# Kernel optimization log

Hardware: AMD Instinct MI355X
Metric: run time of the kernel (lower is better)

Reference implementation:

```python
import jax, jax.numpy as jnp
import numpy as np

BS, LQ = 16, 300
D, NH = 256, 8
HD = D // NH
NLAYERS, DFF = 6, 1024
NLVL, NPTS = 4, 4
SUMP = NLVL * NPTS  # total sampling points per head
SPATIAL = [(80, 80), (40, 40), (20, 20), (10, 10)]
LEN_V = sum(h * w for h, w in SPATIAL)  # 8500
OFFSET_SCALE = 0.5


def layer_norm(x, g, b, eps=1e-5):
    m = jnp.mean(x, -1, keepdims=True)
    v = jnp.mean((x - m) ** 2, -1, keepdims=True)
    return (x - m) * jax.lax.rsqrt(v + eps) * g + b


def bilinear_gather(v, loc, Hs, Ws):
    # v: [bs, nh, Hs*Ws, hd]; loc: [bs, nh, N, 2] in [0,1] (x, y)
    # grid_sample bilinear, align_corners=False, zero padding
    x = loc[..., 0] * Ws - 0.5
    y = loc[..., 1] * Hs - 0.5
    x0 = jnp.floor(x); y0 = jnp.floor(y)
    x1 = x0 + 1.0; y1 = y0 + 1.0
    wx1 = x - x0; wx0 = 1.0 - wx1
    wy1 = y - y0; wy0 = 1.0 - wy1

    def corner(xi, yi, w):
        valid = (xi >= 0) & (xi <= Ws - 1) & (yi >= 0) & (yi <= Hs - 1)
        idx = (jnp.clip(yi, 0, Hs - 1) * Ws + jnp.clip(xi, 0, Ws - 1)).astype(jnp.int32)
        g = jnp.take_along_axis(v, idx[..., None], axis=2)  # [bs,nh,N,hd]
        return g * (w * valid)[..., None]

    return (corner(x0, y0, wx0 * wy0) + corner(x1, y0, wx1 * wy0)
            + corner(x0, y1, wx0 * wy1) + corner(x1, y1, wx1 * wy1))


def ms_deform_attn(value, loc, attn_w):
    # value [bs,LenV,D]; loc [bs,Lq,nh,SUMP,2]; attn_w [bs,Lq,nh,SUMP]
    bs, Lq = loc.shape[:2]
    v = value.reshape(bs, -1, NH, HD).transpose(0, 2, 1, 3)  # [bs,nh,LenV,hd]
    sizes = [h * w for h, w in SPATIAL]
    offs = np.cumsum([0] + sizes)
    outs = []
    for lvl, (Hs, Ws) in enumerate(SPATIAL):
        v_l = v[:, :, offs[lvl]:offs[lvl + 1], :]
        loc_l = loc[:, :, :, lvl * NPTS:(lvl + 1) * NPTS, :]
        loc_l = loc_l.transpose(0, 2, 1, 3, 4).reshape(bs, NH, Lq * NPTS, 2)
        s = bilinear_gather(v_l, loc_l, Hs, Ws).reshape(bs, NH, Lq, NPTS, HD)
        outs.append(s)
    samp = jnp.concatenate(outs, axis=3)  # [bs,nh,Lq,SUMP,hd]
    w = attn_w.transpose(0, 2, 1, 3)[..., None]
    out = jnp.sum(samp * w, axis=3)  # [bs,nh,Lq,hd]
    return out.transpose(0, 2, 1, 3).reshape(bs, Lq, D)


def mha(q_in, k_in, v_in, Wqkv, bqkv, Wo, bo):
    # torch nn.MultiheadAttention (batch_first), no dropout, no mask
    bs, Lq, _ = q_in.shape
    Wq, Wk, Wv = jnp.split(Wqkv, 3, axis=0)
    bq, bk, bv = jnp.split(bqkv, 3)
    q = (q_in @ Wq.T + bq).reshape(bs, Lq, NH, HD)
    k = (k_in @ Wk.T + bk).reshape(bs, -1, NH, HD)
    v = (v_in @ Wv.T + bv).reshape(bs, -1, NH, HD)
    scores = jnp.einsum('bqhd,bkhd->bhqk', q, k) / jnp.sqrt(jnp.float32(HD))
    a = jax.nn.softmax(scores, axis=-1)
    o = jnp.einsum('bhqk,bkhd->bqhd', a, v).reshape(bs, Lq, D)
    return o @ Wo.T + bo


def _forward(target, reference_points, value, query_pos_embed,
             attn_Wqkv, attn_bqkv, attn_Wo, attn_bo, n1_g, n1_b,
             so_W, so_b, aw_W, aw_b, g_W, g_b, gn_g, gn_b,
             l1_W, l1_b, l2_W, l2_b, n3_g, n3_b):
    bs, Lq = target.shape[:2]
    # num_points_scale = 1/n_points per point (all levels use NPTS points)
    nps = jnp.full((SUMP, 1), 1.0 / NPTS, dtype=target.dtype)
    t = target
    for i in range(NLAYERS):
        # self-attention
        q = t + query_pos_embed
        t2 = mha(q, q, t, attn_Wqkv[i], attn_bqkv[i], attn_Wo[i], attn_bo[i])
        t = layer_norm(t + t2, n1_g[i], n1_b[i])
        # MS deformable cross-attention (4-dim reference_points branch)
        qc = t + query_pos_embed
        so = (qc @ so_W[i].T + so_b[i]).reshape(bs, Lq, NH, SUMP, 2)
        aw = jax.nn.softmax((qc @ aw_W[i].T + aw_b[i]).reshape(bs, Lq, NH, SUMP), axis=-1)
        ref = reference_points[:, :, None, None, :]  # [bs,Lq,1,1,4]
        loc = ref[..., :2] + so * nps * ref[..., 2:] * OFFSET_SCALE
        t2 = ms_deform_attn(value, loc, aw)
        # gateway fusion
        gates = jax.nn.sigmoid(jnp.concatenate([t, t2], -1) @ g_W[i].T + g_b[i])
        g1, g2 = jnp.split(gates, 2, axis=-1)
        t = layer_norm(g1 * t + g2 * t2, gn_g[i], gn_b[i])
        # FFN
        t2 = jax.nn.relu(t @ l1_W[i].T + l1_b[i]) @ l2_W[i].T + l2_b[i]
        t = layer_norm(jnp.clip(t + t2, -65504.0, 65504.0), n3_g[i], n3_b[i])
    return t


def setup_inputs() -> dict:
    key = jax.random.key(0)
    ks = iter(jax.random.split(key, 40))

    def rn(shape, s=0.02):
        return jax.random.normal(next(ks), shape, dtype=jnp.float32) * s

    inp = {
        'target': jax.random.normal(next(ks), (BS, LQ, D), dtype=jnp.float32),
        'reference_points': jax.random.uniform(next(ks), (BS, LQ, 4), dtype=jnp.float32) * 0.5 + 0.25,
        'value': jax.random.normal(next(ks), (BS, LEN_V, D), dtype=jnp.float32),
        'query_pos_embed': jax.random.normal(next(ks), (BS, LQ, D), dtype=jnp.float32),
        'attn_Wqkv': rn((NLAYERS, 3 * D, D)),
        'attn_bqkv': jnp.zeros((NLAYERS, 3 * D), jnp.float32),
        'attn_Wo': rn((NLAYERS, D, D)),
        'attn_bo': jnp.zeros((NLAYERS, D), jnp.float32),
        'n1_g': jnp.ones((NLAYERS, D), jnp.float32),
        'n1_b': jnp.zeros((NLAYERS, D), jnp.float32),
        'so_W': rn((NLAYERS, NH * SUMP * 2, D)),
        'so_b': rn((NLAYERS, NH * SUMP * 2), 0.5),
        'aw_W': rn((NLAYERS, NH * SUMP, D)),
        'aw_b': jnp.zeros((NLAYERS, NH * SUMP), jnp.float32),
        'g_W': rn((NLAYERS, 2 * D, 2 * D)),
        'g_b': jnp.zeros((NLAYERS, 2 * D), jnp.float32),
        'gn_g': jnp.ones((NLAYERS, D), jnp.float32),
        'gn_b': jnp.zeros((NLAYERS, D), jnp.float32),
        'l1_W': rn((NLAYERS, DFF, D)),
        'l1_b': jnp.zeros((NLAYERS, DFF), jnp.float32),
        'l2_W': rn((NLAYERS, D, DFF)),
        'l2_b': jnp.zeros((NLAYERS, D), jnp.float32),
        'n3_g': jnp.ones((NLAYERS, D), jnp.float32),
        'n3_b': jnp.zeros((NLAYERS, D), jnp.float32),
    }
    return inp


def reference(target, reference_points, value, query_pos_embed,
              attn_Wqkv, attn_bqkv, attn_Wo, attn_bo, n1_g, n1_b,
              so_W, so_b, aw_W, aw_b, g_W, g_b, gn_g, gn_b,
              l1_W, l1_b, l2_W, l2_b, n3_g, n3_b):
    return _forward(target, reference_points, value, query_pos_embed,
                    attn_Wqkv, attn_bqkv, attn_Wo, attn_bo, n1_g, n1_b,
                    so_W, so_b, aw_W, aw_b, g_W, g_b, gn_g, gn_b,
                    l1_W, l1_b, l2_W, l2_b, n3_g, n3_b)
```

## Files before the change

kernel.cpp:

```cpp
#include <hip/hip_runtime.h>

#define BS 16
#define LQ 300
#define D 256
#define NH 8
#define HD 32
#define DFF 1024
#define ROWS (BS*LQ)
#define LEN_V 8500

typedef __attribute__((ext_vector_type(8))) short short8;
typedef __attribute__((ext_vector_type(4))) float f32x4;

__device__ __forceinline__ uint32_t bf16r(float x)
{
    const uint32_t u = __float_as_uint(x);
    return (u + 0x7fffu + ((u >> 16) & 1u)) >> 16;
}
__device__ __forceinline__ float lof(uint32_t p) { return __uint_as_float(p << 16); }
__device__ __forceinline__ float hif(uint32_t p) { return __uint_as_float(p & 0xffff0000u); }

template<int ACT>
__global__ __launch_bounds__(256)
void gemm_mfma(const float* __restrict__ A, int lda,
               const float* __restrict__ A2, int lda2, int ksplit,
               const float* __restrict__ W,
               const float* __restrict__ bias,
               float* __restrict__ C, int ldc, int coff,
               int K)
{
    __shared__ __align__(16) unsigned short As[64*64];
    __shared__ __align__(16) unsigned short Bs[64*64];
    const int tid  = threadIdx.x;
    const int bm   = blockIdx.x, bn = blockIdx.y;
    const int lane = tid & 63;
    const int w    = tid >> 6;
    const int wm   = (w >> 1) * 32, wn = (w & 1) * 32;
    const int fr   = lane & 15;
    const int fq   = lane >> 4;

    const int srow = tid >> 2;
    const int sg   = tid & 3;

    f32x4 acc[2][2] = {};

    for (int k0 = 0; k0 < K; k0 += 64) {
        float4 a0[2], a1[2], w0[2], w1[2];
#pragma unroll
        for (int p = 0; p < 2; ++p) {
            const int grp = sg + 4*p;
            const int kg  = k0 + grp*8;
            const float* Asrc = (A2 != nullptr && kg >= ksplit)
                ? (A2 + (size_t)(bm*64 + srow)*lda2 + (kg - ksplit))
                : (A  + (size_t)(bm*64 + srow)*lda  + kg);
            a0[p] = *reinterpret_cast<const float4*>(Asrc);
            a1[p] = *reinterpret_cast<const float4*>(Asrc + 4);
            const float* Wsrc = W + (size_t)(bn*64 + srow)*K + kg;
            w0[p] = *reinterpret_cast<const float4*>(Wsrc);
            w1[p] = *reinterpret_cast<const float4*>(Wsrc + 4);
        }
        __syncthreads();
#pragma unroll
        for (int p = 0; p < 2; ++p) {
            const int grp  = sg + 4*p;
            const int slot = grp ^ (srow & 7);
            uint32_t pk[4];
            pk[0] = bf16r(a0[p].x) | (bf16r(a0[p].y) << 16);
            pk[1] = bf16r(a0[p].z) | (bf16r(a0[p].w) << 16);
            pk[2] = bf16r(a1[p].x) | (bf16r(a1[p].y) << 16);
            pk[3] = bf16r(a1[p].z) | (bf16r(a1[p].w) << 16);
            *reinterpret_cast<uint4*>(&As[srow*64 + slot*8]) =
                make_uint4(pk[0], pk[1], pk[2], pk[3]);
            pk[0] = bf16r(w0[p].x) | (bf16r(w0[p].y) << 16);
            pk[1] = bf16r(w0[p].z) | (bf16r(w0[p].w) << 16);
            pk[2] = bf16r(w1[p].x) | (bf16r(w1[p].y) << 16);
            pk[3] = bf16r(w1[p].z) | (bf16r(w1[p].w) << 16);
            *reinterpret_cast<uint4*>(&Bs[srow*64 + slot*8]) =
                make_uint4(pk[0], pk[1], pk[2], pk[3]);
        }
        __syncthreads();
#pragma unroll
        for (int ks = 0; ks < 2; ++ks) {
            short8 af[2], bf[2];
#pragma unroll
            for (int fm = 0; fm < 2; ++fm) {
                const int row = wm + fm*16 + fr;
                const int slot = (ks*4 + fq) ^ (row & 7);
                af[fm] = *reinterpret_cast<const short8*>(&As[row*64 + slot*8]);
            }
#pragma unroll
            for (int fn = 0; fn < 2; ++fn) {
                const int row = wn + fn*16 + fr;
                const int slot = (ks*4 + fq) ^ (row & 7);
                bf[fn] = *reinterpret_cast<const short8*>(&Bs[row*64 + slot*8]);
            }
#pragma unroll
            for (int fm = 0; fm < 2; ++fm)
#pragma unroll
                for (int fn = 0; fn < 2; ++fn)
                    acc[fm][fn] = __builtin_amdgcn_mfma_f32_16x16x32_bf16(
                        af[fm], bf[fn], acc[fm][fn], 0, 0, 0);
        }
    }

#pragma unroll
    for (int fm = 0; fm < 2; ++fm)
#pragma unroll
        for (int fn = 0; fn < 2; ++fn) {
            const int col = bn*64 + wn + fn*16 + fr;
            const float bia = bias[col];
#pragma unroll
            for (int r = 0; r < 4; ++r) {
                const int row = bm*64 + wm + fm*16 + fq*4 + r;
                float v = acc[fm][fn][r] + bia;
                if (ACT == 1) v = fmaxf(v, 0.f);
                if (ACT == 2) v = 1.f / (1.f + __expf(-v));
                C[(size_t)row*ldc + coff + col] = v;
            }
        }
}

__global__ __launch_bounds__(256)
void add_pos(const float* __restrict__ t, const float* __restrict__ pos,
             float* __restrict__ q)
{
    const size_t idx = (size_t)blockIdx.x*256 + threadIdx.x;
    q[idx] = t[idx] + pos[idx];
}

__global__ __launch_bounds__(256)
void mha_block(const float* __restrict__ qkv, float* __restrict__ o)
{
    const int blk = blockIdx.x;
    const int quarter = blk & 3;
    const int bh = blk >> 2;
    const int b = bh >> 3, h = bh & 7;
    const int tid = threadIdx.x;
    const int lane = tid & 63;
    const int w = tid >> 6;

    __shared__ uint32_t Kp[16][320];
    __shared__ uint32_t Vp[150][32];
    __shared__ float    ws[4][304];
    const float* base = qkv + (size_t)b * LQ * 768;
    const int hc = h * 32;

    for (int idx = tid; idx < 300*16; idx += 256) {
        const int j = idx >> 4, d2 = idx & 15;
        const float2 kv = *reinterpret_cast<const float2*>(base + (size_t)j*768 + 256 + hc + 2*d2);
        Kp[d2][j] = (bf16r(kv.y) << 16) | bf16r(kv.x);
    }
    for (int idx = tid; idx < 16*20; idx += 256)
        Kp[idx/20][300 + idx%20] = 0;
    for (int idx = tid; idx < 150*32; idx += 256) {
        const int jp = idx >> 5, d = idx & 31;
        const float lo = base[(size_t)(2*jp  )*768 + 512 + hc + d];
        const float hi = base[(size_t)(2*jp+1)*768 + 512 + hc + d];
        Vp[jp][d] = (bf16r(hi) << 16) | bf16r(lo);
    }
    __syncthreads();

    const float scale = 0.17677669529663687f;
    const int qbase = quarter * 75;
    for (int il = w; il < 75; il += 4) {
        const int iq = qbase + il;
        const float2* qrow = reinterpret_cast<const float2*>(base + (size_t)iq*768 + hc);

        float s0=0.f, s1=0.f, s2=0.f, s3=0.f, s4=0.f;
#pragma unroll
        for (int d2 = 0; d2 < 16; ++d2) {
            const float2 q2 = qrow[d2];
            uint32_t k;
            k = Kp[d2][lane      ]; s0 += lof(k)*q2.x + hif(k)*q2.y;
            k = Kp[d2][lane +  64]; s1 += lof(k)*q2.x + hif(k)*q2.y;
            k = Kp[d2][lane + 128]; s2 += lof(k)*q2.x + hif(k)*q2.y;
            k = Kp[d2][lane + 192]; s3 += lof(k)*q2.x + hif(k)*q2.y;
            k = Kp[d2][lane + 256]; s4 += lof(k)*q2.x + hif(k)*q2.y;
        }
        s0 *= scale; s1 *= scale; s2 *= scale; s3 *= scale;
        s4 = (lane < 44) ? s4*scale : -3e38f;

        float m = fmaxf(fmaxf(fmaxf(s0,s1), fmaxf(s2,s3)), s4);
#pragma unroll
        for (int off = 32; off; off >>= 1) m = fmaxf(m, __shfl_xor(m, off));
        const float e0 = __expf(s0-m), e1 = __expf(s1-m), e2 = __expf(s2-m), e3 = __expf(s3-m);
        const float e4 = (lane < 44) ? __expf(s4-m) : 0.f;
        float sum = e0+e1+e2+e3+e4;
#pragma unroll
        for (int off = 32; off; off >>= 1) sum += __shfl_xor(sum, off);
        const float inv = 1.f / sum;
        ws[w][lane      ] = e0;
        ws[w][lane +  64] = e1;
        ws[w][lane + 128] = e2;
        ws[w][lane + 192] = e3;
        if (lane < 44) ws[w][lane + 256] = e4;

        const int half = lane >> 5, d = lane & 31;
        float acc = 0.f;
#pragma unroll 5
        for (int jp = half*75; jp < half*75 + 75; ++jp) {
            const float2 w2 = *reinterpret_cast<const float2*>(&ws[w][2*jp]);
            const uint32_t v2 = Vp[jp][d];
            acc += lof(v2)*w2.x + hif(v2)*w2.y;
        }
        acc += __shfl_down(acc, 32);
        if (lane < 32)
            o[((size_t)(b*LQ + iq))*256 + hc + d] = acc * inv;
    }
}

__device__ __forceinline__ float blk_sum(float v, float* red)
{
#pragma unroll
    for (int off = 32; off; off >>= 1) v += __shfl_down(v, off, 64);
    const int lane = threadIdx.x & 63, w = threadIdx.x >> 6;
    if (lane == 0) red[w] = v;
    __syncthreads();
    const float s = red[0] + red[1] + red[2] + red[3];
    __syncthreads();
    return s;
}

__global__ __launch_bounds__(256)
void ln_res_pos(const float* __restrict__ t, const float* __restrict__ t2,
                const float* __restrict__ g, const float* __restrict__ bb,
                const float* __restrict__ pos,
                float* __restrict__ t_out, float* __restrict__ q_out)
{
    __shared__ float red[4];
    const size_t idx = (size_t)blockIdx.x*256 + threadIdx.x;
    const float x = t[idx] + t2[idx];
    const float mean = blk_sum(x, red) * (1.f/256.f);
    const float c = x - mean;
    const float var = blk_sum(c*c, red) * (1.f/256.f);
    const float y = c * rsqrtf(var + 1e-5f) * g[threadIdx.x] + bb[threadIdx.x];
    t_out[idx] = y;
    q_out[idx] = y + pos[idx];
}

__global__ __launch_bounds__(256)
void gate_ln(const float* __restrict__ t, const float* __restrict__ t2,
             const float* __restrict__ gates,
             const float* __restrict__ g, const float* __restrict__ bb,
             float* __restrict__ t_out)
{
    __shared__ float red[4];
    const int row = blockIdx.x, dd = threadIdx.x;
    const size_t idx = (size_t)row*256 + dd;
    const float g1 = gates[(size_t)row*512 + dd];
    const float g2 = gates[(size_t)row*512 + 256 + dd];
    const float x = g1 * t[idx] + g2 * t2[idx];
    const float mean = blk_sum(x, red) * (1.f/256.f);
    const float c = x - mean;
    const float var = blk_sum(c*c, red) * (1.f/256.f);
    t_out[idx] = c * rsqrtf(var + 1e-5f) * g[dd] + bb[dd];
}

__global__ __launch_bounds__(256)
void ln_clip(const float* __restrict__ t, const float* __restrict__ t2,
             const float* __restrict__ g, const float* __restrict__ bb,
             float* __restrict__ outp)
{
    __shared__ float red[4];
    const size_t idx = (size_t)blockIdx.x*256 + threadIdx.x;
    float x = t[idx] + t2[idx];
    x = fminf(fmaxf(x, -65504.f), 65504.f);
    const float mean = blk_sum(x, red) * (1.f/256.f);
    const float c = x - mean;
    const float var = blk_sum(c*c, red) * (1.f/256.f);
    outp[idx] = c * rsqrtf(var + 1e-5f) * g[threadIdx.x] + bb[threadIdx.x];
}

__global__ __launch_bounds__(128)
void aw_softmax(float* __restrict__ aw)
{
    const int bq = blockIdx.x;
    const int tid = threadIdx.x;
    const float v = aw[(size_t)bq*128 + tid];
    float m = v;
#pragma unroll
    for (int off = 8; off; off >>= 1) m = fmaxf(m, __shfl_xor(m, off, 16));
    const float e = __expf(v - m);
    float s = e;
#pragma unroll
    for (int off = 8; off; off >>= 1) s += __shfl_xor(s, off, 16);
    aw[(size_t)bq*128 + tid] = e / s;
}

__global__ __launch_bounds__(256)
void deform_attn(const float* __restrict__ value, const float* __restrict__ refp,
                 const float* __restrict__ so, const float* __restrict__ aw,
                 float* __restrict__ outp)
{
    const int bq = blockIdx.x;
    const int b  = bq / LQ;
    const int tid = threadIdx.x;
    __shared__ int   s_idx[128][4];
    __shared__ float s_w[128][4];
    if (tid < 128) {
        const int hp = tid;
        const int p  = hp & 15;
        const int lvl = p >> 2;
        const float Wl = (lvl == 0) ? 80.f : (lvl == 1) ? 40.f : (lvl == 2) ? 20.f : 10.f;
        const float Hl = Wl;
        const int off  = (lvl == 0) ? 0 : (lvl == 1) ? 6400 : (lvl == 2) ? 8000 : 8400;
        const float cx = refp[bq*4+0], cy = refp[bq*4+1];
        const float rw = refp[bq*4+2], rh = refp[bq*4+3];
        const float lx = cx + so[(size_t)bq*256 + hp*2 + 0] * rw * 0.125f;
        const float ly = cy + so[(size_t)bq*256 + hp*2 + 1] * rh * 0.125f;
        const float x = lx * Wl - 0.5f;
        const float y = ly * Hl - 0.5f;
        const float x0 = floorf(x), y0 = floorf(y);
        const float wx1 = x - x0, wx0 = 1.f - wx1;
        const float wy1 = y - y0, wy0 = 1.f - wy1;
        const float a = aw[(size_t)bq*128 + hp];
        const float xs[2]  = {x0, x0 + 1.f}, ys[2]  = {y0, y0 + 1.f};
        const float wxs[2] = {wx0, wx1},     wys[2] = {wy0, wy1};
#pragma unroll
        for (int cyi = 0; cyi < 2; ++cyi)
#pragma unroll
            for (int cxi = 0; cxi < 2; ++cxi) {
                const float xi = xs[cxi], yi = ys[cyi];
                const bool valid = (xi >= 0.f) && (xi <= Wl - 1.f) &&
                                   (yi >= 0.f) && (yi <= Hl - 1.f);
                const float xc = fminf(fmaxf(xi, 0.f), Wl - 1.f);
                const float yc = fminf(fmaxf(yi, 0.f), Hl - 1.f);
                const int c = cyi*2 + cxi;
                s_idx[hp][c] = (int)(yc*Wl + xc) + off;
                s_w[hp][c]   = valid ? (wxs[cxi]*wys[cyi]*a) : 0.f;
            }
    }
    __syncthreads();
    const int h = tid >> 5, d = tid & 31;
    const int col = h*32 + d;
    const float* vb = value + (size_t)b * LEN_V * 256;
    float acc = 0.f;
#pragma unroll
    for (int p = 0; p < 16; ++p) {
        const int hp = (h << 4) | p;
#pragma unroll
        for (int c = 0; c < 4; ++c)
            acc += s_w[hp][c] * vb[(size_t)s_idx[hp][c]*256 + col];
    }
    outp[(size_t)bq*256 + col] = acc;
}

extern "C" void kernel_launch(void* const* d_in, const int* in_sizes, int n_in,
                              void* d_out, int out_size, void* d_ws, size_t ws_size,
                              hipStream_t stream)
{
    (void)in_sizes; (void)n_in; (void)out_size; (void)ws_size;
    const float* target = (const float*)d_in[0];
    const float* refp   = (const float*)d_in[1];
    const float* value  = (const float*)d_in[2];
    const float* qpos   = (const float*)d_in[3];
    const float* Wqkv   = (const float*)d_in[4];
    const float* bqkv   = (const float*)d_in[5];
    const float* Wo     = (const float*)d_in[6];
    const float* bo     = (const float*)d_in[7];
    const float* n1g    = (const float*)d_in[8];
    const float* n1b    = (const float*)d_in[9];
    const float* soW    = (const float*)d_in[10];
    const float* sob    = (const float*)d_in[11];
    const float* awW    = (const float*)d_in[12];
    const float* awb    = (const float*)d_in[13];
    const float* gW     = (const float*)d_in[14];
    const float* gb     = (const float*)d_in[15];
    const float* gng    = (const float*)d_in[16];
    const float* gnb    = (const float*)d_in[17];
    const float* l1W    = (const float*)d_in[18];
    const float* l1b    = (const float*)d_in[19];
    const float* l2W    = (const float*)d_in[20];
    const float* l2b    = (const float*)d_in[21];
    const float* n3g    = (const float*)d_in[22];
    const float* n3b    = (const float*)d_in[23];

    float* p = (float*)d_ws;
    float* t_buf = p;  p += (size_t)ROWS*D;
    float* q_buf = p;  p += (size_t)ROWS*D;
    float* qkv   = p;
    float* o_buf = qkv + (size_t)ROWS*768;
    float* hid   = qkv;
    p += (size_t)ROWS*(768 + 256);
    float* t2    = p;  p += (size_t)ROWS*D;
    float* so_b  = p;  p += (size_t)ROWS*D;
    float* aw_b  = p;  p += (size_t)ROWS*128;
    float* gates = p;  p += (size_t)ROWS*512;

    hipMemcpyAsync(t_buf, target, (size_t)ROWS*D*sizeof(float),
                   hipMemcpyDeviceToDevice, stream);

    for (int i = 0; i < 6; ++i) {
        const float* Wqkv_i = Wqkv + (size_t)i*768*256;
        const float* bqkv_i = bqkv + (size_t)i*768;
        const float* Wo_i   = Wo   + (size_t)i*256*256;
        const float* bo_i   = bo   + (size_t)i*256;
        const float* n1g_i  = n1g  + (size_t)i*256;
        const float* n1b_i  = n1b  + (size_t)i*256;
        const float* soW_i  = soW  + (size_t)i*256*256;
        const float* sob_i  = sob  + (size_t)i*256;
        const float* awW_i  = awW  + (size_t)i*128*256;
        const float* awb_i  = awb  + (size_t)i*128;
        const float* gW_i   = gW   + (size_t)i*512*512;
        const float* gb_i   = gb   + (size_t)i*512;
        const float* gng_i  = gng  + (size_t)i*256;
        const float* gnb_i  = gnb  + (size_t)i*256;
        const float* l1W_i  = l1W  + (size_t)i*1024*256;
        const float* l1b_i  = l1b  + (size_t)i*1024;
        const float* l2W_i  = l2W  + (size_t)i*256*1024;
        const float* l2b_i  = l2b  + (size_t)i*256;
        const float* n3g_i  = n3g  + (size_t)i*256;
        const float* n3b_i  = n3b  + (size_t)i*256;

        add_pos<<<ROWS, 256, 0, stream>>>(t_buf, qpos, q_buf);
        gemm_mfma<0><<<dim3(75, 8), 256, 0, stream>>>(q_buf, 256, nullptr, 0, 0,
            Wqkv_i, bqkv_i, qkv, 768, 0, 256);
        gemm_mfma<0><<<dim3(75, 4), 256, 0, stream>>>(t_buf, 256, nullptr, 0, 0,
            Wqkv_i + 512*256, bqkv_i + 512, qkv, 768, 512, 256);
        mha_block<<<BS*NH*4, 256, 0, stream>>>(qkv, o_buf);
        gemm_mfma<0><<<dim3(75, 4), 256, 0, stream>>>(o_buf, 256, nullptr, 0, 0,
            Wo_i, bo_i, t2, 256, 0, 256);
        ln_res_pos<<<ROWS, 256, 0, stream>>>(t_buf, t2, n1g_i, n1b_i, qpos, t_buf, q_buf);

        gemm_mfma<0><<<dim3(75, 4), 256, 0, stream>>>(q_buf, 256, nullptr, 0, 0,
            soW_i, sob_i, so_b, 256, 0, 256);
        gemm_mfma<0><<<dim3(75, 2), 256, 0, stream>>>(q_buf, 256, nullptr, 0, 0,
            awW_i, awb_i, aw_b, 128, 0, 256);
        aw_softmax<<<ROWS, 128, 0, stream>>>(aw_b);
        deform_attn<<<ROWS, 256, 0, stream>>>(value, refp, so_b, aw_b, t2);

        gemm_mfma<2><<<dim3(75, 8), 256, 0, stream>>>(t_buf, 256, t2, 256, 256,
            gW_i, gb_i, gates, 512, 0, 512);
        gate_ln<<<ROWS, 256, 0, stream>>>(t_buf, t2, gates, gng_i, gnb_i, t_buf);

        gemm_mfma<1><<<dim3(75, 16), 256, 0, stream>>>(t_buf, 256, nullptr, 0, 0,
            l1W_i, l1b_i, hid, 1024, 0, 256);
        gemm_mfma<0><<<dim3(75, 4), 256, 0, stream>>>(hid, 1024, nullptr, 0, 0,
            l2W_i, l2b_i, t2, 256, 0, 1024);
        ln_clip<<<ROWS, 256, 0, stream>>>(t_buf, t2, n3g_i, n3b_i,
                                          (i == 5) ? (float*)d_out : t_buf);
    }
}
```

Before: 1.396 ms.

## Pre-convert weights to bf16 once and fuse offset/attention-weight GEMMs with softmax

All layer weight matrices are converted to bf16 once per call into workspace, so the GEMM kernel loads half the weight bytes and skips per-tile conversion. The sampling-offset and attention-weight projections are merged into one GEMM writing a 384-wide buffer with a split bias. The softmax moves into the deformable attention kernel, removing a separate launch. In exchange there are seven conversion launches per call and a larger workspace.

```diff
diff --git a/kernel.cpp b/kernel.cpp
--- a/kernel.cpp
+++ b/kernel.cpp
@@ -11,6 +11,7 @@
 
 typedef __attribute__((ext_vector_type(8))) short short8;
 typedef __attribute__((ext_vector_type(4))) float f32x4;
+typedef unsigned short ushort_t;
 
 __device__ __forceinline__ uint32_t bf16r(float x)
 {
@@ -22,15 +23,14 @@
 
 template<int ACT>
 __global__ __launch_bounds__(256)
-void gemm_mfma(const float* __restrict__ A, int lda,
-               const float* __restrict__ A2, int lda2, int ksplit,
-               const float* __restrict__ W,
-               const float* __restrict__ bias,
-               float* __restrict__ C, int ldc, int coff,
-               int K)
-{
-    __shared__ __align__(16) unsigned short As[64*64];
-    __shared__ __align__(16) unsigned short Bs[64*64];
+void gemm_aw(const float* __restrict__ A, int lda,
+             const float* __restrict__ A2, int lda2, int ksplit,
+             const ushort_t* __restrict__ W,
+             const float* __restrict__ bias, const float* __restrict__ bias2, int bsplit,
+             float* __restrict__ C, int ldc, int coff, int K)
+{
+    __shared__ __align__(16) ushort_t As[64*64];
+    __shared__ __align__(16) ushort_t Bs[64*64];
     const int tid  = threadIdx.x;
     const int bm   = blockIdx.x, bn = blockIdx.y;
     const int lane = tid & 63;
@@ -45,25 +45,23 @@
     f32x4 acc[2][2] = {};
 
     for (int k0 = 0; k0 < K; k0 += 64) {
-        float4 a0[2], a1[2], w0[2], w1[2];
+        float4 a0[2], a1[2];
+        uint4  wv[2];
 #pragma unroll
         for (int p = 0; p < 2; ++p) {
-            const int grp = sg + 4*p;
-            const int kg  = k0 + grp*8;
+            const int slot = sg + 4*p;
+            const int kg   = k0 + slot*8;
             const float* Asrc = (A2 != nullptr && kg >= ksplit)
                 ? (A2 + (size_t)(bm*64 + srow)*lda2 + (kg - ksplit))
                 : (A  + (size_t)(bm*64 + srow)*lda  + kg);
             a0[p] = *reinterpret_cast<const float4*>(Asrc);
             a1[p] = *reinterpret_cast<const float4*>(Asrc + 4);
-            const float* Wsrc = W + (size_t)(bn*64 + srow)*K + kg;
-            w0[p] = *reinterpret_cast<const float4*>(Wsrc);
-            w1[p] = *reinterpret_cast<const float4*>(Wsrc + 4);
+            wv[p] = *reinterpret_cast<const uint4*>(W + (size_t)(bn*64 + srow)*K + kg);
         }
         __syncthreads();
 #pragma unroll
         for (int p = 0; p < 2; ++p) {
-            const int grp  = sg + 4*p;
-            const int slot = grp ^ (srow & 7);
+            const int slot = (sg + 4*p) ^ (srow & 7);
             uint32_t pk[4];
             pk[0] = bf16r(a0[p].x) | (bf16r(a0[p].y) << 16);
             pk[1] = bf16r(a0[p].z) | (bf16r(a0[p].w) << 16);
@@ -71,12 +69,7 @@
             pk[3] = bf16r(a1[p].z) | (bf16r(a1[p].w) << 16);
             *reinterpret_cast<uint4*>(&As[srow*64 + slot*8]) =
                 make_uint4(pk[0], pk[1], pk[2], pk[3]);
-            pk[0] = bf16r(w0[p].x) | (bf16r(w0[p].y) << 16);
-            pk[1] = bf16r(w0[p].z) | (bf16r(w0[p].w) << 16);
-            pk[2] = bf16r(w1[p].x) | (bf16r(w1[p].y) << 16);
-            pk[3] = bf16r(w1[p].z) | (bf16r(w1[p].w) << 16);
-            *reinterpret_cast<uint4*>(&Bs[srow*64 + slot*8]) =
-                make_uint4(pk[0], pk[1], pk[2], pk[3]);
+            *reinterpret_cast<uint4*>(&Bs[srow*64 + slot*8]) = wv[p];
         }
         __syncthreads();
 #pragma unroll
@@ -108,7 +101,8 @@
 #pragma unroll
         for (int fn = 0; fn < 2; ++fn) {
             const int col = bn*64 + wn + fn*16 + fr;
-            const float bia = bias[col];
+            const float bia = (bias2 != nullptr && col >= bsplit)
+                            ? bias2[col - bsplit] : bias[col];
 #pragma unroll
             for (int r = 0; r < 4; ++r) {
                 const int row = bm*64 + wm + fm*16 + fq*4 + r;
@@ -118,6 +112,17 @@
                 C[(size_t)row*ldc + coff + col] = v;
             }
         }
+}
+
+__global__ __launch_bounds__(256)
+void cvt_strided(const float* __restrict__ src, ushort_t* __restrict__ dst,
+                 int per_layer, int dst_stride, int dst_off, int nlayers)
+{
+    const int total = per_layer * nlayers;
+    for (int i = blockIdx.x*256 + threadIdx.x; i < total; i += gridDim.x*256) {
+        const int l = i / per_layer, r = i - l*per_layer;
+        dst[(size_t)l*dst_stride + dst_off + r] = (ushort_t)bf16r(src[i]);
+    }
 }
 
 __global__ __launch_bounds__(256)
@@ -271,26 +276,9 @@
     outp[idx] = c * rsqrtf(var + 1e-5f) * g[threadIdx.x] + bb[threadIdx.x];
 }
 
-__global__ __launch_bounds__(128)
-void aw_softmax(float* __restrict__ aw)
-{
-    const int bq = blockIdx.x;
-    const int tid = threadIdx.x;
-    const float v = aw[(size_t)bq*128 + tid];
-    float m = v;
-#pragma unroll
-    for (int off = 8; off; off >>= 1) m = fmaxf(m, __shfl_xor(m, off, 16));
-    const float e = __expf(v - m);
-    float s = e;
-#pragma unroll
-    for (int off = 8; off; off >>= 1) s += __shfl_xor(s, off, 16);
-    aw[(size_t)bq*128 + tid] = e / s;
-}
-
 __global__ __launch_bounds__(256)
 void deform_attn(const float* __restrict__ value, const float* __restrict__ refp,
-                 const float* __restrict__ so, const float* __restrict__ aw,
-                 float* __restrict__ outp)
+                 const float* __restrict__ soaw, float* __restrict__ outp)
 {
     const int bq = blockIdx.x;
     const int b  = bq / LQ;
@@ -304,16 +292,25 @@
         const float Wl = (lvl == 0) ? 80.f : (lvl == 1) ? 40.f : (lvl == 2) ? 20.f : 10.f;
         const float Hl = Wl;
         const int off  = (lvl == 0) ? 0 : (lvl == 1) ? 6400 : (lvl == 2) ? 8000 : 8400;
+        const float logit = soaw[(size_t)bq*384 + 256 + hp];
+        float m = logit;
+#pragma unroll
+        for (int o = 8; o; o >>= 1) m = fmaxf(m, __shfl_xor(m, o, 16));
+        const float e = __expf(logit - m);
+        float ssum = e;
+#pragma unroll
+        for (int o = 8; o; o >>= 1) ssum += __shfl_xor(ssum, o, 16);
+        const float a = e / ssum;
+
         const float cx = refp[bq*4+0], cy = refp[bq*4+1];
         const float rw = refp[bq*4+2], rh = refp[bq*4+3];
-        const float lx = cx + so[(size_t)bq*256 + hp*2 + 0] * rw * 0.125f;
-        const float ly = cy + so[(size_t)bq*256 + hp*2 + 1] * rh * 0.125f;
+        const float lx = cx + soaw[(size_t)bq*384 + hp*2    ] * rw * 0.125f;
+        const float ly = cy + soaw[(size_t)bq*384 + hp*2 + 1] * rh * 0.125f;
         const float x = lx * Wl - 0.5f;
         const float y = ly * Hl - 0.5f;
         const float x0 = floorf(x), y0 = floorf(y);
         const float wx1 = x - x0, wx0 = 1.f - wx1;
         const float wy1 = y - y0, wy0 = 1.f - wy1;
-        const float a = aw[(size_t)bq*128 + hp];
         const float xs[2]  = {x0, x0 + 1.f}, ys[2]  = {y0, y0 + 1.f};
         const float wxs[2] = {wx0, wx1},     wys[2] = {wy0, wy1};
 #pragma unroll
@@ -383,60 +380,72 @@
     float* hid   = qkv;
     p += (size_t)ROWS*(768 + 256);
     float* t2    = p;  p += (size_t)ROWS*D;
-    float* so_b  = p;  p += (size_t)ROWS*D;
-    float* aw_b  = p;  p += (size_t)ROWS*128;
+    float* soaw  = p;  p += (size_t)ROWS*384;
     float* gates = p;  p += (size_t)ROWS*512;
+    ushort_t* w_bf = (ushort_t*)p;
+
+    ushort_t* wqkv_bf = w_bf;
+    ushort_t* wo_bf   = wqkv_bf + 6*196608;
+    ushort_t* wsoaw_bf= wo_bf   + 6*65536;
+    ushort_t* wg_bf   = wsoaw_bf+ 6*98304;
+    ushort_t* wl1_bf  = wg_bf   + 6*262144;
+    ushort_t* wl2_bf  = wl1_bf  + 6*262144;
+
+    cvt_strided<<<1024, 256, 0, stream>>>(Wqkv, wqkv_bf, 196608, 196608, 0, 6);
+    cvt_strided<<<512,  256, 0, stream>>>(Wo,   wo_bf,   65536,  65536,  0, 6);
+    cvt_strided<<<512,  256, 0, stream>>>(soW,  wsoaw_bf,65536,  98304,  0, 6);
+    cvt_strided<<<256,  256, 0, stream>>>(awW,  wsoaw_bf,32768,  98304,  65536, 6);
+    cvt_strided<<<1024, 256, 0, stream>>>(gW,   wg_bf,   262144, 262144, 0, 6);
+    cvt_strided<<<1024, 256, 0, stream>>>(l1W,  wl1_bf,  262144, 262144, 0, 6);
+    cvt_strided<<<1024, 256, 0, stream>>>(l2W,  wl2_bf,  262144, 262144, 0, 6);
 
     hipMemcpyAsync(t_buf, target, (size_t)ROWS*D*sizeof(float),
                    hipMemcpyDeviceToDevice, stream);
 
     for (int i = 0; i < 6; ++i) {
-        const float* Wqkv_i = Wqkv + (size_t)i*768*256;
         const float* bqkv_i = bqkv + (size_t)i*768;
-        const float* Wo_i   = Wo   + (size_t)i*256*256;
         const float* bo_i   = bo   + (size_t)i*256;
         const float* n1g_i  = n1g  + (size_t)i*256;
         const float* n1b_i  = n1b  + (size_t)i*256;
-        const float* soW_i  = soW  + (size_t)i*256*256;
         const float* sob_i  = sob  + (size_t)i*256;
-        const float* awW_i  = awW  + (size_t)i*128*256;
         const float* awb_i  = awb  + (size_t)i*128;
-        const float* gW_i   = gW   + (size_t)i*512*512;
         const float* gb_i   = gb   + (size_t)i*512;
         const float* gng_i  = gng  + (size_t)i*256;
         const float* gnb_i  = gnb  + (size_t)i*256;
-        const float* l1W_i  = l1W  + (size_t)i*1024*256;
         const float* l1b_i  = l1b  + (size_t)i*1024;
-        const float* l2W_i  = l2W  + (size_t)i*256*1024;
         const float* l2b_i  = l2b  + (size_t)i*256;
         const float* n3g_i  = n3g  + (size_t)i*256;
         const float* n3b_i  = n3b  + (size_t)i*256;
 
+        const ushort_t* wqkv_i = wqkv_bf  + (size_t)i*196608;
+        const ushort_t* wo_i   = wo_bf    + (size_t)i*65536;
+        const ushort_t* wsa_i  = wsoaw_bf + (size_t)i*98304;
+        const ushort_t* wg_i   = wg_bf    + (size_t)i*262144;
+        const ushort_t* wl1_i  = wl1_bf   + (size_t)i*262144;
+        const ushort_t* wl2_i  = wl2_bf   + (size_t)i*262144;
+
         add_pos<<<ROWS, 256, 0, stream>>>(t_buf, qpos, q_buf);
-        gemm_mfma<0><<<dim3(75, 8), 256, 0, stream>>>(q_buf, 256, nullptr, 0, 0,
-            Wqkv_i, bqkv_i, qkv, 768, 0, 256);
-        gemm_mfma<0><<<dim3(75, 4), 256, 0, stream>>>(t_buf, 256, nullptr, 0, 0,
-            Wqkv_i + 512*256, bqkv_i + 512, qkv, 768, 512, 256);
+        gemm_aw<0><<<dim3(75, 8), 256, 0, stream>>>(q_buf, 256, nullptr, 0, 0,
+            wqkv_i, bqkv_i, nullptr, 0, qkv, 768, 0, 256);
+        gemm_aw<0><<<dim3(75, 4), 256, 0, stream>>>(t_buf, 256, nullptr, 0, 0,
+            wqkv_i + 512*256, bqkv_i + 512, nullptr, 0, qkv, 768, 512, 256);
         mha_block<<<BS*NH*4, 256, 0, stream>>>(qkv, o_buf);
-        gemm_mfma<0><<<dim3(75, 4), 256, 0, stream>>>(o_buf, 256, nullptr, 0, 0,
-            Wo_i, bo_i, t2, 256, 0, 256);
+        gemm_aw<0><<<dim3(75, 4), 256, 0, stream>>>(o_buf, 256, nullptr, 0, 0,
+            wo_i, bo_i, nullptr, 0, t2, 256, 0, 256);
         ln_res_pos<<<ROWS, 256, 0, stream>>>(t_buf, t2, n1g_i, n1b_i, qpos, t_buf, q_buf);
 
-        gemm_mfma<0><<<dim3(75, 4), 256, 0, stream>>>(q_buf, 256, nullptr, 0, 0,
-            soW_i, sob_i, so_b, 256, 0, 256);
-        gemm_mfma<0><<<dim3(75, 2), 256, 0, stream>>>(q_buf, 256, nullptr, 0, 0,
-            awW_i, awb_i, aw_b, 128, 0, 256);
-        aw_softmax<<<ROWS, 128, 0, stream>>>(aw_b);
-        deform_attn<<<ROWS, 256, 0, stream>>>(value, refp, so_b, aw_b, t2);
-
-        gemm_mfma<2><<<dim3(75, 8), 256, 0, stream>>>(t_buf, 256, t2, 256, 256,
-            gW_i, gb_i, gates, 512, 0, 512);
+        gemm_aw<0><<<dim3(75, 6), 256, 0, stream>>>(q_buf, 256, nullptr, 0, 0,
+            wsa_i, sob_i, awb_i, 256, soaw, 384, 0, 256);
+        deform_attn<<<ROWS, 256, 0, stream>>>(value, refp, soaw, t2);
+
+        gemm_aw<2><<<dim3(75, 8), 256, 0, stream>>>(t_buf, 256, t2, 256, 256,
+            wg_i, gb_i, nullptr, 0, gates, 512, 0, 512);
         gate_ln<<<ROWS, 256, 0, stream>>>(t_buf, t2, gates, gng_i, gnb_i, t_buf);
 
-        gemm_mfma<1><<<dim3(75, 16), 256, 0, stream>>>(t_buf, 256, nullptr, 0, 0,
-            l1W_i, l1b_i, hid, 1024, 0, 256);
-        gemm_mfma<0><<<dim3(75, 4), 256, 0, stream>>>(hid, 1024, nullptr, 0, 0,
-            l2W_i, l2b_i, t2, 256, 0, 1024);
+        gemm_aw<1><<<dim3(75, 16), 256, 0, stream>>>(t_buf, 256, nullptr, 0, 0,
+            wl1_i, l1b_i, nullptr, 0, hid, 1024, 0, 256);
+        gemm_aw<0><<<dim3(75, 4), 256, 0, stream>>>(hid, 1024, nullptr, 0, 0,
+            wl2_i, l2b_i, nullptr, 0, t2, 256, 0, 1024);
         ln_clip<<<ROWS, 256, 0, stream>>>(t_buf, t2, n3g_i, n3b_i,
                                           (i == 5) ? (float*)d_out : t_buf);
     }
```

After: 1.673 ms. 1.2x slower.

## Fuse GEMM launches, softmax into deform_attn, and pos-add into layernorms

Applied to the files above, without the earlier changes.

The two QKV GEMMs become one launch that switches the A operand by column-block. The sampling-offset and attention-weight GEMMs become one launch that switches weights and outputs by column-block. The softmax kernel is folded into deform_attn, and the query+pos add moves into ln_clip and a prep kernel that also replaces the initial memcpy. This removes several kernel launches and intermediate global round-trips per layer, at the cost of some extra per-block branching in the GEMM.

```diff
diff --git a/kernel.cpp b/kernel.cpp
--- a/kernel.cpp
+++ b/kernel.cpp
@@ -22,12 +22,13 @@
 
 template<int ACT>
 __global__ __launch_bounds__(256)
-void gemm_mfma(const float* __restrict__ A, int lda,
-               const float* __restrict__ A2, int lda2, int ksplit,
-               const float* __restrict__ W,
-               const float* __restrict__ bias,
-               float* __restrict__ C, int ldc, int coff,
-               int K)
+void gemm_f32(const float* __restrict__ A, const float* __restrict__ Aalt,
+              int bnsplit_a, int lda,
+              const float* __restrict__ A2, int lda2, int ksplit,
+              const float* __restrict__ W, const float* __restrict__ W2, int bnw,
+              const float* __restrict__ bias, const float* __restrict__ bias2,
+              float* __restrict__ C, int ldc, float* __restrict__ C2, int ldc2,
+              int K)
 {
     __shared__ __align__(16) unsigned short As[64*64];
     __shared__ __align__(16) unsigned short Bs[64*64];
@@ -42,28 +43,37 @@
     const int srow = tid >> 2;
     const int sg   = tid & 3;
 
+    if (bn >= bnsplit_a) A = Aalt;
+    const float* Wb; const float* biasb; float* Cb; int ldcb; int colbase;
+    if (bn < bnw) {
+        Wb = W  + (size_t)bn*64*K;        biasb = bias;
+        Cb = C;  ldcb = ldc;  colbase = bn*64;
+    } else {
+        Wb = W2 + (size_t)(bn-bnw)*64*K;  biasb = bias2;
+        Cb = C2; ldcb = ldc2; colbase = (bn-bnw)*64;
+    }
+
     f32x4 acc[2][2] = {};
 
     for (int k0 = 0; k0 < K; k0 += 64) {
         float4 a0[2], a1[2], w0[2], w1[2];
 #pragma unroll
         for (int p = 0; p < 2; ++p) {
-            const int grp = sg + 4*p;
-            const int kg  = k0 + grp*8;
+            const int slot = sg + 4*p;
+            const int kg   = k0 + slot*8;
             const float* Asrc = (A2 != nullptr && kg >= ksplit)
                 ? (A2 + (size_t)(bm*64 + srow)*lda2 + (kg - ksplit))
                 : (A  + (size_t)(bm*64 + srow)*lda  + kg);
             a0[p] = *reinterpret_cast<const float4*>(Asrc);
             a1[p] = *reinterpret_cast<const float4*>(Asrc + 4);
-            const float* Wsrc = W + (size_t)(bn*64 + srow)*K + kg;
+            const float* Wsrc = Wb + (size_t)srow*K + kg;
             w0[p] = *reinterpret_cast<const float4*>(Wsrc);
             w1[p] = *reinterpret_cast<const float4*>(Wsrc + 4);
         }
         __syncthreads();
 #pragma unroll
         for (int p = 0; p < 2; ++p) {
-            const int grp  = sg + 4*p;
-            const int slot = grp ^ (srow & 7);
+            const int slot = (sg + 4*p) ^ (srow & 7);
             uint32_t pk[4];
             pk[0] = bf16r(a0[p].x) | (bf16r(a0[p].y) << 16);
             pk[1] = bf16r(a0[p].z) | (bf16r(a0[p].w) << 16);
@@ -107,25 +117,27 @@
     for (int fm = 0; fm < 2; ++fm)
 #pragma unroll
         for (int fn = 0; fn < 2; ++fn) {
-            const int col = bn*64 + wn + fn*16 + fr;
-            const float bia = bias[col];
+            const int coll = wn + fn*16 + fr;
+            const float bia = biasb[colbase + coll];
 #pragma unroll
             for (int r = 0; r < 4; ++r) {
                 const int row = bm*64 + wm + fm*16 + fq*4 + r;
                 float v = acc[fm][fn][r] + bia;
                 if (ACT == 1) v = fmaxf(v, 0.f);
                 if (ACT == 2) v = 1.f / (1.f + __expf(-v));
-                C[(size_t)row*ldc + coff + col] = v;
+                Cb[(size_t)row*ldcb + colbase + coll] = v;
             }
         }
 }
 
 __global__ __launch_bounds__(256)
-void add_pos(const float* __restrict__ t, const float* __restrict__ pos,
-             float* __restrict__ q)
+void prep0(const float* __restrict__ target, const float* __restrict__ pos,
+           float* __restrict__ t, float* __restrict__ q)
 {
     const size_t idx = (size_t)blockIdx.x*256 + threadIdx.x;
-    q[idx] = t[idx] + pos[idx];
+    const float v = target[idx];
+    t[idx] = v;
+    q[idx] = v + pos[idx];
 }
 
 __global__ __launch_bounds__(256)
@@ -259,7 +271,8 @@
 __global__ __launch_bounds__(256)
 void ln_clip(const float* __restrict__ t, const float* __restrict__ t2,
              const float* __restrict__ g, const float* __restrict__ bb,
-             float* __restrict__ outp)
+             const float* __restrict__ pos,
+             float* __restrict__ outp, float* __restrict__ q_out)
 {
     __shared__ float red[4];
     const size_t idx = (size_t)blockIdx.x*256 + threadIdx.x;
@@ -268,28 +281,14 @@
     const float mean = blk_sum(x, red) * (1.f/256.f);
     const float c = x - mean;
     const float var = blk_sum(c*c, red) * (1.f/256.f);
-    outp[idx] = c * rsqrtf(var + 1e-5f) * g[threadIdx.x] + bb[threadIdx.x];
-}
-
-__global__ __launch_bounds__(128)
-void aw_softmax(float* __restrict__ aw)
-{
-    const int bq = blockIdx.x;
-    const int tid = threadIdx.x;
-    const float v = aw[(size_t)bq*128 + tid];
-    float m = v;
-#pragma unroll
-    for (int off = 8; off; off >>= 1) m = fmaxf(m, __shfl_xor(m, off, 16));
-    const float e = __expf(v - m);
-    float s = e;
-#pragma unroll
-    for (int off = 8; off; off >>= 1) s += __shfl_xor(s, off, 16);
-    aw[(size_t)bq*128 + tid] = e / s;
+    const float y = c * rsqrtf(var + 1e-5f) * g[threadIdx.x] + bb[threadIdx.x];
+    outp[idx] = y;
+    if (q_out != nullptr) q_out[idx] = y + pos[idx];
 }
 
 __global__ __launch_bounds__(256)
 void deform_attn(const float* __restrict__ value, const float* __restrict__ refp,
-                 const float* __restrict__ so, const float* __restrict__ aw,
+                 const float* __restrict__ so, const float* __restrict__ awl,
                  float* __restrict__ outp)
 {
     const int bq = blockIdx.x;
@@ -304,16 +303,25 @@
         const float Wl = (lvl == 0) ? 80.f : (lvl == 1) ? 40.f : (lvl == 2) ? 20.f : 10.f;
         const float Hl = Wl;
         const int off  = (lvl == 0) ? 0 : (lvl == 1) ? 6400 : (lvl == 2) ? 8000 : 8400;
+        const float logit = awl[(size_t)bq*128 + hp];
+        float m = logit;
+#pragma unroll
+        for (int o = 8; o; o >>= 1) m = fmaxf(m, __shfl_xor(m, o, 16));
+        const float e = __expf(logit - m);
+        float ssum = e;
+#pragma unroll
+        for (int o = 8; o; o >>= 1) ssum += __shfl_xor(ssum, o, 16);
+        const float a = e / ssum;
+
         const float cx = refp[bq*4+0], cy = refp[bq*4+1];
         const float rw = refp[bq*4+2], rh = refp[bq*4+3];
-        const float lx = cx + so[(size_t)bq*256 + hp*2 + 0] * rw * 0.125f;
+        const float lx = cx + so[(size_t)bq*256 + hp*2    ] * rw * 0.125f;
         const float ly = cy + so[(size_t)bq*256 + hp*2 + 1] * rh * 0.125f;
         const float x = lx * Wl - 0.5f;
         const float y = ly * Hl - 0.5f;
         const float x0 = floorf(x), y0 = floorf(y);
         const float wx1 = x - x0, wx0 = 1.f - wx1;
         const float wy1 = y - y0, wy0 = 1.f - wy1;
-        const float a = aw[(size_t)bq*128 + hp];
         const float xs[2]  = {x0, x0 + 1.f}, ys[2]  = {y0, y0 + 1.f};
         const float wxs[2] = {wx0, wx1},     wys[2] = {wy0, wy1};
 #pragma unroll
@@ -387,8 +395,7 @@
     float* aw_b  = p;  p += (size_t)ROWS*128;
     float* gates = p;  p += (size_t)ROWS*512;
 
-    hipMemcpyAsync(t_buf, target, (size_t)ROWS*D*sizeof(float),
-                   hipMemcpyDeviceToDevice, stream);
+    prep0<<<ROWS, 256, 0, stream>>>(target, qpos, t_buf, q_buf);
 
     for (int i = 0; i < 6; ++i) {
         const float* Wqkv_i = Wqkv + (size_t)i*768*256;
@@ -412,32 +419,39 @@
         const float* n3g_i  = n3g  + (size_t)i*256;
         const float* n3b_i  = n3b  + (size_t)i*256;
 
-        add_pos<<<ROWS, 256, 0, stream>>>(t_buf, qpos, q_buf);
-        gemm_mfma<0><<<dim3(75, 8), 256, 0, stream>>>(q_buf, 256, nullptr, 0, 0,
-            Wqkv_i, bqkv_i, qkv, 768, 0, 256);
-        gemm_mfma<0><<<dim3(75, 4), 256, 0, stream>>>(t_buf, 256, nullptr, 0, 0,
-            Wqkv_i + 512*256, bqkv_i + 512, qkv, 768, 512, 256);
+        gemm_f32<0><<<dim3(75, 12), 256, 0, stream>>>(
+            q_buf, t_buf, 8, 256,  nullptr, 0, 0,
+            Wqkv_i, nullptr, 999,  bqkv_i, nullptr,
+            qkv, 768, nullptr, 0,  256);
         mha_block<<<BS*NH*4, 256, 0, stream>>>(qkv, o_buf);
-        gemm_mfma<0><<<dim3(75, 4), 256, 0, stream>>>(o_buf, 256, nullptr, 0, 0,
-            Wo_i, bo_i, t2, 256, 0, 256);
+        gemm_f32<0><<<dim3(75, 4), 256, 0, stream>>>(
+            o_buf, o_buf, 999, 256,  nullptr, 0, 0,
+            Wo_i, nullptr, 999,  bo_i, nullptr,
+            t2, 256, nullptr, 0,  256);
         ln_res_pos<<<ROWS, 256, 0, stream>>>(t_buf, t2, n1g_i, n1b_i, qpos, t_buf, q_buf);
 
-        gemm_mfma<0><<<dim3(75, 4), 256, 0, stream>>>(q_buf, 256, nullptr, 0, 0,
-            soW_i, sob_i, so_b, 256, 0, 256);
-        gemm_mfma<0><<<dim3(75, 2), 256, 0, stream>>>(q_buf, 256, nullptr, 0, 0,
-            awW_i, awb_i, aw_b, 128, 0, 256);
-        aw_softmax<<<ROWS, 128, 0, stream>>>(aw_b);
+        gemm_f32<0><<<dim3(75, 6), 256, 0, stream>>>(
+            q_buf, q_buf, 999, 256,  nullptr, 0, 0,
+            soW_i, awW_i, 4,  sob_i, awb_i,
+            so_b, 256, aw_b, 128,  256);
         deform_attn<<<ROWS, 256, 0, stream>>>(value, refp, so_b, aw_b, t2);
 
-        gemm_mfma<2><<<dim3(75, 8), 256, 0, stream>>>(t_buf, 256, t2, 256, 256,
-            gW_i, gb_i, gates, 512, 0, 512);
+        gemm_f32<2><<<dim3(75, 8), 256, 0, stream>>>(
+            t_buf, t_buf, 999, 256,  t2, 256, 256,
+            gW_i, nullptr, 999,  gb_i, nullptr,
+            gates, 512, nullptr, 0,  512);
         gate_ln<<<ROWS, 256, 0, stream>>>(t_buf, t2, gates, gng_i, gnb_i, t_buf);
 
-        gemm_mfma<1><<<dim3(75, 16), 256, 0, stream>>>(t_buf, 256, nullptr, 0, 0,
-            l1W_i, l1b_i, hid, 1024, 0, 256);
-        gemm_mfma<0><<<dim3(75, 4), 256, 0, stream>>>(hid, 1024, nullptr, 0, 0,
-            l2W_i, l2b_i, t2, 256, 0, 1024);
-        ln_clip<<<ROWS, 256, 0, stream>>>(t_buf, t2, n3g_i, n3b_i,
-                                          (i == 5) ? (float*)d_out : t_buf);
-    }
-}
+        gemm_f32<1><<<dim3(75, 16), 256, 0, stream>>>(
+            t_buf, t_buf, 999, 256,  nullptr, 0, 0,
+            l1W_i, nullptr, 999,  l1b_i, nullptr,
+            hid, 1024, nullptr, 0,  256);
+        gemm_f32<0><<<dim3(75, 4), 256, 0, stream>>>(
+            hid, hid, 999, 1024,  nullptr, 0, 0,
+            l2W_i, nullptr, 999,  l2b_i, nullptr,
+            t2, 256, nullptr, 0,  1024);
+        ln_clip<<<ROWS, 256, 0, stream>>>(t_buf, t2, n3g_i, n3b_i, qpos,
+                                          (i == 5) ? (float*)d_out : t_buf,
+                                          (i < 5) ? q_buf : nullptr);
+    }
+}
```

Result: faster. 1.309 ms (-6.3%).
